# Performance work log

Measured on AMD Instinct MI355X. Metric: run time of the kernel, lower is better.

The kernel has to match this reference:

```python
import jax, jax.numpy as jnp
import numpy as np

N_OSC = 256
BATCH = 1024
DT = 0.1
STEPS = 10


def setup_inputs() -> dict:
    key = jax.random.key(0)
    k_theta, k_K, k_omega = jax.random.split(key, 3)
    theta_init = jax.random.normal(k_theta, (BATCH, N_OSC), dtype=jnp.float32)
    K0 = jax.random.normal(k_K, (N_OSC, N_OSC), dtype=jnp.float32) * 0.1
    K = (K0 + K0.T) / 2  # symmetric coupling matrix, as in torch init
    omega = jax.random.normal(k_omega, (N_OSC,), dtype=jnp.float32) * 0.1
    K_global = jnp.float32(0.5)
    return {"theta_init": theta_init, "K": K, "omega": omega, "K_global": K_global}


def reference(theta_init, K, omega, K_global):
    n = K.shape[0]

    def step(theta, _):
        # diff[b, i, j] = theta[b, j] - theta[b, i]
        diff = theta[..., None, :] - theta[..., :, None]
        coupling_sum = jnp.sum(K * jnp.sin(diff), axis=-1)  # (batch, n)
        dtheta = omega + (K_global / n) * coupling_sum
        theta_new = theta + DT * dtheta
        # wrap to (-pi, pi]
        theta_new = jnp.arctan2(jnp.sin(theta_new), jnp.cos(theta_new))
        return theta_new, None

    theta, _ = jax.lax.scan(step, theta_init, None, length=STEPS)
    cos_mean = jnp.cos(theta).mean(axis=-1)
    sin_mean = jnp.sin(theta).mean(axis=-1)
    coherence = jnp.sqrt(cos_mean ** 2 + sin_mean ** 2)
    return theta, coherence
```

## Files before the change

### kernel.cpp

```cpp
#include <hip/hip_runtime.h>
#include <math.h>


typedef __attribute__((ext_vector_type(4))) float f32x4;
typedef __attribute__((ext_vector_type(2))) long long2_t;

constexpr int N       = 256;
constexpr int RB      = 16;
constexpr int STEPS   = 10;
constexpr int WAVES   = 8;
constexpr int THREADS = WAVES * 64;
constexpr float DT    = 0.1f;
constexpr float TWO_PI     = 6.28318530717958648f;
constexpr float INV_TWO_PI = 0.15915494309189535f;

__global__ __launch_bounds__(512)
void pack_k(const float* __restrict__ Kmat, unsigned char* __restrict__ kf8)
{
    const int id   = blockIdx.x * blockDim.x + threadIdx.x;
    const int T    = id >> 9;
    const int c    = (id >> 6) & 7;
    const int lane = id & 63;
    const int q    = lane >> 4, l15 = lane & 15;
    const float* src = Kmat + (size_t)(16 * T + l15) * N + 32 * c + 8 * q;
    float4 lo = *(const float4*)src;
    float4 hi = *(const float4*)(src + 4);
    int w0 = __builtin_amdgcn_cvt_pk_fp8_f32(lo.x, lo.y, 0, false);
    w0     = __builtin_amdgcn_cvt_pk_fp8_f32(lo.z, lo.w, w0, true);
    int w1 = __builtin_amdgcn_cvt_pk_fp8_f32(hi.x, hi.y, 0, false);
    w1     = __builtin_amdgcn_cvt_pk_fp8_f32(hi.z, hi.w, w1, true);
    int2 out; out.x = w0; out.y = w1;
    *(int2*)(kf8 + (size_t)id * 8) = out;
}

__global__ __launch_bounds__(THREADS, 2)
void kuramoto_r6(const float* __restrict__ theta0,
                 const unsigned char* __restrict__ kf8,
                 const float* __restrict__ omega,
                 const float* __restrict__ kglob,
                 float* __restrict__ theta_out,
                 float* __restrict__ coh_out)
{
    __shared__ __align__(16) unsigned char SC[2][RB * 512];
    __shared__ float redS[RB][WAVES], redC[RB][WAVES];

    const int tid  = threadIdx.x;
    const int wv   = tid >> 6;
    const int lane = tid & 63;
    const int q    = lane >> 4;
    const int l15  = lane & 15;
    const int b0   = blockIdx.x * RB;

    const float kgn = kglob[0] * (1.0f / 256.0f);

    long kf[2][8];
#pragma unroll
    for (int t = 0; t < 2; ++t) {
        const unsigned char* base = kf8 + (size_t)((2 * wv + t) * 512 + lane) * 8;
#pragma unroll
        for (int c = 0; c < 8; ++c)
            kf[t][c] = *(const long*)(base + (size_t)c * 512);
    }

    float th[8], om[8], sn[8], cs[8];
#pragma unroll
    for (int t = 0; t < 2; ++t) {
        const int ob = 32 * wv + 16 * t + 4 * q;
        float4 t4 = *(const float4*)(theta0 + (size_t)(b0 + l15) * N + ob);
        float4 o4 = *(const float4*)(omega + ob);
        th[4*t+0] = t4.x; th[4*t+1] = t4.y; th[4*t+2] = t4.z; th[4*t+3] = t4.w;
        om[4*t+0] = o4.x; om[4*t+1] = o4.y; om[4*t+2] = o4.z; om[4*t+3] = o4.w;
    }
#pragma unroll
    for (int k = 0; k < 8; ++k)
        __sincosf(th[k], &sn[k], &cs[k]);

    const int so = 4 * (q & 1);
    const int g0 = 4 * wv + (q >> 1);

    for (int s = 0; s < STEPS; ++s) {
        unsigned char* rowp = &SC[s & 1][l15 * 512];
#pragma unroll
        for (int t = 0; t < 2; ++t) {
            int spk = __builtin_amdgcn_cvt_pk_fp8_f32(sn[4*t+0], sn[4*t+1], 0, false);
            spk     = __builtin_amdgcn_cvt_pk_fp8_f32(sn[4*t+2], sn[4*t+3], spk, true);
            int cpk = __builtin_amdgcn_cvt_pk_fp8_f32(cs[4*t+0], cs[4*t+1], 0, false);
            cpk     = __builtin_amdgcn_cvt_pk_fp8_f32(cs[4*t+2], cs[4*t+3], cpk, true);
            const int base = (((g0 + 2 * t) ^ l15) << 4);
            *(int*)(rowp + base + so)     = spk;
            *(int*)(rowp + base + 8 + so) = cpk;
        }
        __syncthreads();

        f32x4 aS[2], aC[2];
        aS[0] = (f32x4){0.f,0.f,0.f,0.f}; aS[1] = (f32x4){0.f,0.f,0.f,0.f};
        aC[0] = (f32x4){0.f,0.f,0.f,0.f}; aC[1] = (f32x4){0.f,0.f,0.f,0.f};
#pragma unroll
        for (int c = 0; c < 8; ++c) {
            long2_t v = *(const long2_t*)(rowp + ((((4 * c + q) ^ l15)) << 4));
            aS[0] = __builtin_amdgcn_mfma_f32_16x16x32_fp8_fp8(kf[0][c], v.x, aS[0], 0, 0, 0);
            aC[0] = __builtin_amdgcn_mfma_f32_16x16x32_fp8_fp8(kf[0][c], v.y, aC[0], 0, 0, 0);
            aS[1] = __builtin_amdgcn_mfma_f32_16x16x32_fp8_fp8(kf[1][c], v.x, aS[1], 0, 0, 0);
            aC[1] = __builtin_amdgcn_mfma_f32_16x16x32_fp8_fp8(kf[1][c], v.y, aC[1], 0, 0, 0);
        }

#pragma unroll
        for (int t = 0; t < 2; ++t)
#pragma unroll
            for (int r = 0; r < 4; ++r) {
                const int k = 4 * t + r;
                float coup = cs[k] * aS[t][r] - sn[k] * aC[t][r];
                float d  = DT * fmaf(kgn, coup, om[k]);
                float d2 = d * d;
                float sd = d * fmaf(d2, -1.0f / 6.0f, 1.0f);
                float cd = fmaf(d2, fmaf(d2, 1.0f / 24.0f, -0.5f), 1.0f);
                float s2 = fmaf(sn[k], cd,  cs[k] * sd);
                float c2 = fmaf(cs[k], cd, -sn[k] * sd);
                sn[k] = s2; cs[k] = c2; th[k] += d;
            }
    }

    float ps = 0.f, pc = 0.f;
#pragma unroll
    for (int t = 0; t < 2; ++t) {
        const int ob = 32 * wv + 16 * t + 4 * q;
        float4 outv;
        outv.x = fmaf(-TWO_PI, rintf(th[4*t+0] * INV_TWO_PI), th[4*t+0]);
        outv.y = fmaf(-TWO_PI, rintf(th[4*t+1] * INV_TWO_PI), th[4*t+1]);
        outv.z = fmaf(-TWO_PI, rintf(th[4*t+2] * INV_TWO_PI), th[4*t+2]);
        outv.w = fmaf(-TWO_PI, rintf(th[4*t+3] * INV_TWO_PI), th[4*t+3]);
        *(float4*)(theta_out + (size_t)(b0 + l15) * N + ob) = outv;
#pragma unroll
        for (int r = 0; r < 4; ++r) { ps += sn[4*t+r]; pc += cs[4*t+r]; }
    }
    ps += __shfl_xor(ps, 16, 64);  pc += __shfl_xor(pc, 16, 64);
    ps += __shfl_xor(ps, 32, 64);  pc += __shfl_xor(pc, 32, 64);
    if (q == 0) { redS[l15][wv] = ps; redC[l15][wv] = pc; }
    __syncthreads();
    if (tid < RB) {
        float S = 0.f, C = 0.f;
#pragma unroll
        for (int k = 0; k < WAVES; ++k) { S += redS[tid][k]; C += redC[tid][k]; }
        float sm = S * (1.0f / 256.0f);
        float cm = C * (1.0f / 256.0f);
        coh_out[b0 + tid] = sqrtf(sm * sm + cm * cm);
    }
}

extern "C" void kernel_launch(void* const* d_in, const int* in_sizes, int n_in,
                              void* d_out, int out_size, void* d_ws, size_t ws_size,
                              hipStream_t stream) {
    const float* theta0 = (const float*)d_in[0];
    const float* Kmat   = (const float*)d_in[1];
    const float* omega  = (const float*)d_in[2];
    const float* kglob  = (const float*)d_in[3];

    unsigned char* kf8 = (unsigned char*)d_ws;

    float* theta_out = (float*)d_out;
    float* coh_out   = theta_out + 1024 * N;

    pack_k<<<dim3(16), dim3(512), 0, stream>>>(Kmat, kf8);
    kuramoto_r6<<<dim3(1024 / RB), dim3(THREADS), 0, stream>>>(
        theta0, kf8, omega, kglob, theta_out, coh_out);
}
```

Baseline: 70.89 us.

## Fuse K fp8 packing into main kernel and restructure step loop pipelining

Result: slower. 74.63 us (+5.3%).

```diff
diff --git a/kernel.cpp b/kernel.cpp
--- a/kernel.cpp
+++ b/kernel.cpp
@@ -14,28 +14,9 @@
 constexpr float TWO_PI     = 6.28318530717958648f;
 constexpr float INV_TWO_PI = 0.15915494309189535f;
 
-__global__ __launch_bounds__(512)
-void pack_k(const float* __restrict__ Kmat, unsigned char* __restrict__ kf8)
-{
-    const int id   = blockIdx.x * blockDim.x + threadIdx.x;
-    const int T    = id >> 9;
-    const int c    = (id >> 6) & 7;
-    const int lane = id & 63;
-    const int q    = lane >> 4, l15 = lane & 15;
-    const float* src = Kmat + (size_t)(16 * T + l15) * N + 32 * c + 8 * q;
-    float4 lo = *(const float4*)src;
-    float4 hi = *(const float4*)(src + 4);
-    int w0 = __builtin_amdgcn_cvt_pk_fp8_f32(lo.x, lo.y, 0, false);
-    w0     = __builtin_amdgcn_cvt_pk_fp8_f32(lo.z, lo.w, w0, true);
-    int w1 = __builtin_amdgcn_cvt_pk_fp8_f32(hi.x, hi.y, 0, false);
-    w1     = __builtin_amdgcn_cvt_pk_fp8_f32(hi.z, hi.w, w1, true);
-    int2 out; out.x = w0; out.y = w1;
-    *(int2*)(kf8 + (size_t)id * 8) = out;
-}
-
 __global__ __launch_bounds__(THREADS, 2)
-void kuramoto_r6(const float* __restrict__ theta0,
-                 const unsigned char* __restrict__ kf8,
+void kuramoto_r7(const float* __restrict__ theta0,
+                 const float* __restrict__ Kmat,
                  const float* __restrict__ omega,
                  const float* __restrict__ kglob,
                  float* __restrict__ theta_out,
@@ -56,10 +37,17 @@
     long kf[2][8];
 #pragma unroll
     for (int t = 0; t < 2; ++t) {
-        const unsigned char* base = kf8 + (size_t)((2 * wv + t) * 512 + lane) * 8;
+        const float* kr = Kmat + (size_t)(16 * (2 * wv + t) + l15) * N + 8 * q;
 #pragma unroll
-        for (int c = 0; c < 8; ++c)
-            kf[t][c] = *(const long*)(base + (size_t)c * 512);
+        for (int c = 0; c < 8; ++c) {
+            float4 lo = *(const float4*)(kr + 32 * c);
+            float4 hi = *(const float4*)(kr + 32 * c + 4);
+            int w0 = __builtin_amdgcn_cvt_pk_fp8_f32(lo.x, lo.y, 0, false);
+            w0     = __builtin_amdgcn_cvt_pk_fp8_f32(lo.z, lo.w, w0, true);
+            int w1 = __builtin_amdgcn_cvt_pk_fp8_f32(hi.x, hi.y, 0, false);
+            w1     = __builtin_amdgcn_cvt_pk_fp8_f32(hi.z, hi.w, w1, true);
+            kf[t][c] = (long)(unsigned)w0 | ((long)w1 << 32);
+        }
     }
 
     float th[8], om[8], sn[8], cs[8];
@@ -78,38 +66,40 @@
     const int so = 4 * (q & 1);
     const int g0 = 4 * wv + (q >> 1);
 
+#pragma unroll
+    for (int t = 0; t < 2; ++t) {
+        int spk = __builtin_amdgcn_cvt_pk_fp8_f32(sn[4*t+0], sn[4*t+1], 0, false);
+        spk     = __builtin_amdgcn_cvt_pk_fp8_f32(sn[4*t+2], sn[4*t+3], spk, true);
+        int cpk = __builtin_amdgcn_cvt_pk_fp8_f32(cs[4*t+0], cs[4*t+1], 0, false);
+        cpk     = __builtin_amdgcn_cvt_pk_fp8_f32(cs[4*t+2], cs[4*t+3], cpk, true);
+        const int base = (((g0 + 2 * t) ^ l15) << 4);
+        *(int*)(&SC[0][l15 * 512] + base + so)     = spk;
+        *(int*)(&SC[0][l15 * 512] + base + 8 + so) = cpk;
+    }
+
     for (int s = 0; s < STEPS; ++s) {
-        unsigned char* rowp = &SC[s & 1][l15 * 512];
+        __syncthreads();
+        const unsigned char* rdp = &SC[s & 1][l15 * 512];
+        unsigned char*       wrp = &SC[(s + 1) & 1][l15 * 512];
+
+        long2_t v[8];
+#pragma unroll
+        for (int c = 0; c < 8; ++c)
+            v[c] = *(const long2_t*)(rdp + ((((4 * c + q) ^ l15)) << 4));
+
 #pragma unroll
         for (int t = 0; t < 2; ++t) {
-            int spk = __builtin_amdgcn_cvt_pk_fp8_f32(sn[4*t+0], sn[4*t+1], 0, false);
-            spk     = __builtin_amdgcn_cvt_pk_fp8_f32(sn[4*t+2], sn[4*t+3], spk, true);
-            int cpk = __builtin_amdgcn_cvt_pk_fp8_f32(cs[4*t+0], cs[4*t+1], 0, false);
-            cpk     = __builtin_amdgcn_cvt_pk_fp8_f32(cs[4*t+2], cs[4*t+3], cpk, true);
-            const int base = (((g0 + 2 * t) ^ l15) << 4);
-            *(int*)(rowp + base + so)     = spk;
-            *(int*)(rowp + base + 8 + so) = cpk;
-        }
-        __syncthreads();
-
-        f32x4 aS[2], aC[2];
-        aS[0] = (f32x4){0.f,0.f,0.f,0.f}; aS[1] = (f32x4){0.f,0.f,0.f,0.f};
-        aC[0] = (f32x4){0.f,0.f,0.f,0.f}; aC[1] = (f32x4){0.f,0.f,0.f,0.f};
+            f32x4 aS = (f32x4){0.f, 0.f, 0.f, 0.f};
+            f32x4 aC = (f32x4){0.f, 0.f, 0.f, 0.f};
 #pragma unroll
-        for (int c = 0; c < 8; ++c) {
-            long2_t v = *(const long2_t*)(rowp + ((((4 * c + q) ^ l15)) << 4));
-            aS[0] = __builtin_amdgcn_mfma_f32_16x16x32_fp8_fp8(kf[0][c], v.x, aS[0], 0, 0, 0);
-            aC[0] = __builtin_amdgcn_mfma_f32_16x16x32_fp8_fp8(kf[0][c], v.y, aC[0], 0, 0, 0);
-            aS[1] = __builtin_amdgcn_mfma_f32_16x16x32_fp8_fp8(kf[1][c], v.x, aS[1], 0, 0, 0);
-            aC[1] = __builtin_amdgcn_mfma_f32_16x16x32_fp8_fp8(kf[1][c], v.y, aC[1], 0, 0, 0);
-        }
-
-#pragma unroll
-        for (int t = 0; t < 2; ++t)
+            for (int c = 0; c < 8; ++c) {
+                aS = __builtin_amdgcn_mfma_f32_16x16x32_fp8_fp8(kf[t][c], v[c].x, aS, 0, 0, 0);
+                aC = __builtin_amdgcn_mfma_f32_16x16x32_fp8_fp8(kf[t][c], v[c].y, aC, 0, 0, 0);
+            }
 #pragma unroll
             for (int r = 0; r < 4; ++r) {
                 const int k = 4 * t + r;
-                float coup = cs[k] * aS[t][r] - sn[k] * aC[t][r];
+                float coup = cs[k] * aS[r] - sn[k] * aC[r];
                 float d  = DT * fmaf(kgn, coup, om[k]);
                 float d2 = d * d;
                 float sd = d * fmaf(d2, -1.0f / 6.0f, 1.0f);
@@ -118,6 +108,14 @@
                 float c2 = fmaf(cs[k], cd, -sn[k] * sd);
                 sn[k] = s2; cs[k] = c2; th[k] += d;
             }
+            int spk = __builtin_amdgcn_cvt_pk_fp8_f32(sn[4*t+0], sn[4*t+1], 0, false);
+            spk     = __builtin_amdgcn_cvt_pk_fp8_f32(sn[4*t+2], sn[4*t+3], spk, true);
+            int cpk = __builtin_amdgcn_cvt_pk_fp8_f32(cs[4*t+0], cs[4*t+1], 0, false);
+            cpk     = __builtin_amdgcn_cvt_pk_fp8_f32(cs[4*t+2], cs[4*t+3], cpk, true);
+            const int base = (((g0 + 2 * t) ^ l15) << 4);
+            *(int*)(wrp + base + so)     = spk;
+            *(int*)(wrp + base + 8 + so) = cpk;
+        }
     }
 
     float ps = 0.f, pc = 0.f;
@@ -155,12 +153,9 @@
     const float* omega  = (const float*)d_in[2];
     const float* kglob  = (const float*)d_in[3];
 
-    unsigned char* kf8 = (unsigned char*)d_ws;
-
     float* theta_out = (float*)d_out;
     float* coh_out   = theta_out + 1024 * N;
 
-    pack_k<<<dim3(16), dim3(512), 0, stream>>>(Kmat, kf8);
-    kuramoto_r6<<<dim3(1024 / RB), dim3(THREADS), 0, stream>>>(
-        theta0, kf8, omega, kglob, theta_out, coh_out);
+    kuramoto_r7<<<dim3(1024 / RB), dim3(THREADS), 0, stream>>>(
+        theta0, Kmat, omega, kglob, theta_out, coh_out);
 }
```
